# Kernel optimization log

Hardware: AMD Instinct MI355X
Metric: run time of the kernel (lower is better)

## Reference

```python
import jax, jax.numpy as jnp
import numpy as np

B, L, D, N, OUT, NL = 4, 1024, 512, 16, 512, 2  # batch, seq, channels, ssm state, output, layers


def setup_inputs() -> dict:
    key = jax.random.key(0)
    ks = jax.random.split(key, 8)
    sc = D ** -0.5
    return {
        "x": jax.random.normal(ks[0], (B, L, D), jnp.float32),
        # diagonal A: negative real part (real_random=False -> stable negative init)
        "A": -jax.random.uniform(ks[1], (NL, D, N), jnp.float32, 0.1, 1.0),
        "D_skip": jnp.ones((NL, D), jnp.float32),
        "WB": jax.random.normal(ks[2], (NL, D, N), jnp.float32) * sc,
        "bB": jnp.zeros((NL, N), jnp.float32),
        "WC": jax.random.normal(ks[3], (NL, D, N), jnp.float32) * sc,
        "bC": jnp.zeros((NL, N), jnp.float32),
        "Wdt": jax.random.normal(ks[4], (NL, D, D), jnp.float32) * sc,
        "bdt": jnp.full((NL, D), -4.0, jnp.float32),  # softplus(-4) ~ 0.018 -> small dt
        "Wlin": jax.random.normal(ks[5], (NL, D, D), jnp.float32) * sc,
        "blin": jnp.zeros((NL, D), jnp.float32),
        "Wdec": jax.random.normal(ks[6], (D, OUT), jnp.float32) * sc,
        "bdec": jnp.zeros((OUT,), jnp.float32),
    }


def _linear_scan(a, b):
    # first-order linear recurrence h_t = a_t * h_{t-1} + b_t via parallel scan
    def comb(c1, c2):
        a1, b1 = c1
        a2, b2 = c2
        return a1 * a2, a2 * b1 + b2
    return jax.lax.associative_scan(comb, (a, b), axis=1)[1]


def _forward(x, A, D_skip, WB, bB, WC, bC, Wdt, bdt, Wlin, blin, Wdec, bdec):
    y = x
    for i in range(NL):
        # selection mechanism: dt, B, C are input-dependent
        dt = jax.nn.softplus(jnp.einsum('bld,de->ble', y, Wdt[i]) + bdt[i])  # (B,L,D)
        Bm = jnp.einsum('bld,dn->bln', y, WB[i]) + bB[i]                      # (B,L,N)
        Cm = jnp.einsum('bld,dn->bln', y, WC[i]) + bC[i]                      # (B,L,N)
        # ZOH discretization of diagonal SSM
        a = jnp.exp(dt[..., None] * A[i])                                     # (B,L,D,N)
        b = (dt * y)[..., None] * Bm[:, :, None, :]                           # (B,L,D,N)
        h = _linear_scan(a, b)                                                # (B,L,D,N)
        out = jnp.einsum('bldn,bln->bld', h, Cm) + D_skip[i] * y
        y = jnp.maximum(out, 0.0)                                             # ReLU
        y = jnp.einsum('bld,de->ble', y, Wlin[i]) + blin[i]                   # per-layer Linear
    return jnp.einsum('bld,do->blo', y, Wdec) + bdec                          # decoder


def reference(x, A, D_skip, WB, bB, WC, bC, Wdt, bdt, Wlin, blin, Wdec, bdec):
    return _forward(x, A, D_skip, WB, bB, WC, bC, Wdt, bdt, Wlin, blin, Wdec, bdec)
```

## Files before the change

### kernel.cpp

```cpp
#include <hip/hip_runtime.h>

#define BQ 4
#define LQ 1024
#define DQ 512
#define NQ 16
#define MQ (BQ*LQ)
#define CHUNK 16
#define NCH (LQ/CHUNK)
#define KQ 512
#define NFUSE 576

typedef __bf16  bf16x8  __attribute__((ext_vector_type(8)));
typedef float   floatx4 __attribute__((ext_vector_type(4)));

__device__ __forceinline__ float softplus_f(float x) {
    return (x > 20.0f) ? x : log1pf(__expf(x));
}
__device__ __forceinline__ unsigned short f2b(float f) {
    union { float f; unsigned u; } x; x.f = f;
    unsigned r = x.u + 0x7fffu + ((x.u >> 16) & 1u);
    return (unsigned short)(r >> 16);
}
__device__ __forceinline__ float b2f(unsigned short u) {
    union { unsigned u; float f; } x; x.u = (unsigned)u << 16;
    return x.f;
}
__device__ __forceinline__ void load_lds16(const void* g, void* l) {
    __builtin_amdgcn_global_load_lds(
        (const __attribute__((address_space(1))) unsigned int*)g,
        (__attribute__((address_space(3))) unsigned int*)l, 16, 0, 0);
}

__device__ __forceinline__ void stage_tile(
    const unsigned short* g, unsigned short* lds, int wave, int lane)
{
    const int rsub = lane >> 3;
    const int gsrc = (lane & 7) ^ rsub;
    #pragma unroll
    for (int j = 0; j < 2; ++j) {
        int rbase = wave * 16 + j * 8;
        load_lds16(g + (size_t)(rbase + rsub) * KQ + gsrc * 8,
                   lds + (size_t)rbase * 64);
    }
}

__device__ __forceinline__ void gemm_db_core(
    const unsigned short* __restrict__ Abf,
    const unsigned short* __restrict__ Wt,
    int bm, int bn,
    unsigned short (*As)[64*64], unsigned short (*Bs)[64*64],
    floatx4 acc[2][2])
{
    const int lane = threadIdx.x & 63, wave = threadIdx.x >> 6;
    const int mw = (wave & 1) * 32, nw = (wave >> 1) * 32;
    const int r15 = lane & 15, q = lane >> 4;
    const int slot0 = q ^ (r15 & 7);

    #pragma unroll
    for (int i = 0; i < 2; ++i)
        #pragma unroll
        for (int j = 0; j < 2; ++j) acc[i][j] = (floatx4){0.f,0.f,0.f,0.f};

    const unsigned short* ga = Abf + (size_t)bm * KQ;
    const unsigned short* gb = Wt  + (size_t)bn * KQ;
    stage_tile(ga, As[0], wave, lane);
    stage_tile(gb, Bs[0], wave, lane);

    #pragma unroll
    for (int it = 0; it < 8; ++it) {
        __syncthreads();
        if (it < 7) {
            stage_tile(ga + (it + 1) * 64, As[(it + 1) & 1], wave, lane);
            stage_tile(gb + (it + 1) * 64, Bs[(it + 1) & 1], wave, lane);
        }
        const unsigned short* a = As[it & 1];
        const unsigned short* b = Bs[it & 1];
        #pragma unroll
        for (int ks = 0; ks < 2; ++ks) {
            int slot = slot0 ^ (ks * 4);
            bf16x8 af0 = *(const bf16x8*)&a[(mw      + r15) * 64 + slot * 8];
            bf16x8 af1 = *(const bf16x8*)&a[(mw + 16 + r15) * 64 + slot * 8];
            bf16x8 bf0 = *(const bf16x8*)&b[(nw      + r15) * 64 + slot * 8];
            bf16x8 bf1 = *(const bf16x8*)&b[(nw + 16 + r15) * 64 + slot * 8];
            acc[0][0] = __builtin_amdgcn_mfma_f32_16x16x32_bf16(af0, bf0, acc[0][0], 0,0,0);
            acc[1][0] = __builtin_amdgcn_mfma_f32_16x16x32_bf16(af1, bf0, acc[1][0], 0,0,0);
            acc[0][1] = __builtin_amdgcn_mfma_f32_16x16x32_bf16(af0, bf1, acc[0][1], 0,0,0);
            acc[1][1] = __builtin_amdgcn_mfma_f32_16x16x32_bf16(af1, bf1, acc[1][1], 0,0,0);
        }
    }
}

__device__ __forceinline__ void write_fused(
    floatx4 acc[2][2], int bm, int bn_local,
    const float* __restrict__ bias,
    unsigned short* __restrict__ dtb, float* __restrict__ Bm, float* __restrict__ Cm)
{
    const int lane = threadIdx.x & 63, wave = threadIdx.x >> 6;
    const int mw = (wave & 1) * 32, nw = (wave >> 1) * 32;
    const int col0 = lane & 15, rq = lane >> 4;
    #pragma unroll
    for (int nt = 0; nt < 2; ++nt) {
        int nb = bn_local + nw + nt * 16;
        int n  = nb + col0;
        if (nb >= 544) continue;
        float bv = bias[n];
        #pragma unroll
        for (int mt = 0; mt < 2; ++mt)
            #pragma unroll
            for (int r = 0; r < 4; ++r) {
                int m = bm + mw + mt * 16 + rq * 4 + r;
                float v = acc[mt][nt][r] + bv;
                if (nb < 512)      dtb[(size_t)m * DQ + n] = f2b(softplus_f(v));
                else if (nb < 528) Bm[(size_t)m * NQ + (n - 512)] = v;
                else               Cm[(size_t)m * NQ + (n - 528)] = v;
            }
    }
}

__global__ __launch_bounds__(256) void gemm_fused0(
    const unsigned short* __restrict__ Abf,
    const unsigned short* __restrict__ Wt,
    const float* __restrict__ bias,
    unsigned short* __restrict__ dtb, float* __restrict__ Bm, float* __restrict__ Cm)
{
    __shared__ __align__(16) unsigned short As[2][64*64];
    __shared__ __align__(16) unsigned short Bs[2][64*64];
    const int bm = blockIdx.x * 64, bn = blockIdx.y * 64;
    floatx4 acc[2][2];
    gemm_db_core(Abf, Wt, bm, bn, As, Bs, acc);
    write_fused(acc, bm, bn, bias, dtb, Bm, Cm);
}

__global__ __launch_bounds__(256) void gemm_pair(
    const unsigned short* __restrict__ Abf,
    const unsigned short* __restrict__ Wt_lin0,
    const unsigned short* __restrict__ Wcomb1,
    const float* __restrict__ blin0, const float* __restrict__ bcomb1,
    unsigned short* __restrict__ y16b,
    unsigned short* __restrict__ dtb1, float* __restrict__ Bm1, float* __restrict__ Cm1)
{
    __shared__ __align__(16) unsigned short As[2][64*64];
    __shared__ __align__(16) unsigned short Bs[2][64*64];
    const int bm = blockIdx.x * 64;
    const int tile = blockIdx.y;
    floatx4 acc[2][2];
    if (tile < 8) {
        const int bn = tile * 64;
        gemm_db_core(Abf, Wt_lin0, bm, bn, As, Bs, acc);
        const int lane = threadIdx.x & 63, wave = threadIdx.x >> 6;
        const int mw = (wave & 1) * 32, nw = (wave >> 1) * 32;
        const int col0 = lane & 15, rq = lane >> 4;
        #pragma unroll
        for (int nt = 0; nt < 2; ++nt) {
            int n = bn + nw + nt * 16 + col0;
            float bv = blin0[n];
            #pragma unroll
            for (int mt = 0; mt < 2; ++mt)
                #pragma unroll
                for (int r = 0; r < 4; ++r) {
                    int m = bm + mw + mt * 16 + rq * 4 + r;
                    y16b[(size_t)m * DQ + n] = f2b(acc[mt][nt][r] + bv);
                }
        }
    } else {
        const int bn = (tile - 8) * 64;
        gemm_db_core(Abf, Wcomb1, bm, bn, As, Bs, acc);
        write_fused(acc, bm, bn, bcomb1, dtb1, Bm1, Cm1);
    }
}

__global__ __launch_bounds__(256) void gemm_final(
    const unsigned short* __restrict__ Abf,
    const unsigned short* __restrict__ Wt,
    const float* __restrict__ bias,
    float* __restrict__ out)
{
    __shared__ __align__(16) unsigned short As[2][64*64];
    __shared__ __align__(16) unsigned short Bs[2][64*64];
    const int bm = blockIdx.x * 64, bn = blockIdx.y * 64;
    floatx4 acc[2][2];
    gemm_db_core(Abf, Wt, bm, bn, As, Bs, acc);
    const int lane = threadIdx.x & 63, wave = threadIdx.x >> 6;
    const int mw = (wave & 1) * 32, nw = (wave >> 1) * 32;
    const int col0 = lane & 15, rq = lane >> 4;
    #pragma unroll
    for (int nt = 0; nt < 2; ++nt) {
        int n = bn + nw + nt * 16 + col0;
        float bv = bias[n];
        #pragma unroll
        for (int mt = 0; mt < 2; ++mt)
            #pragma unroll
            for (int r = 0; r < 4; ++r) {
                int m = bm + mw + mt * 16 + rq * 4 + r;
                out[(size_t)m * DQ + n] = acc[mt][nt][r] + bv;
            }
    }
}

__global__ __launch_bounds__(256) void prep_all(
    const float* __restrict__ Wdt, const float* __restrict__ Wlin,
    const float* __restrict__ Wdec,
    const float* __restrict__ WB, const float* __restrict__ WC,
    const float* __restrict__ x,
    unsigned short* __restrict__ Wf0, unsigned short* __restrict__ Wf1,
    unsigned short* __restrict__ Wt_lin0, unsigned short* __restrict__ Wdec_t,
    unsigned short* __restrict__ Wlin0_o, unsigned short* __restrict__ Wlin1_o,
    unsigned short* __restrict__ y16)
{
    const int bid = blockIdx.x, tid = threadIdx.x;
    if (bid < 1024) {
        __shared__ float tile[32][33];
        int mat = bid >> 8, t = bid & 255;
        const float* src; unsigned short* dst;
        switch (mat) {
            case 0:  src = Wdt;                  dst = Wf0;     break;
            case 1:  src = Wdt + (size_t)KQ*KQ;  dst = Wf1;     break;
            case 2:  src = Wlin;                 dst = Wt_lin0; break;
            default: src = Wdec;                 dst = Wdec_t;  break;
        }
        int bx = (t & 15) * 32, by = (t >> 4) * 32;
        int tx = tid & 31, ty = tid >> 5;
        #pragma unroll
        for (int i = 0; i < 32; i += 8)
            tile[ty + i][tx] = src[(size_t)(bx + ty + i) * KQ + by + tx];
        __syncthreads();
        #pragma unroll
        for (int i = 0; i < 32; i += 8)
            dst[(size_t)(by + ty + i) * KQ + bx + tx] = f2b(tile[tx][ty + i]);
    } else if (bid < 1536) {
        int q = bid - 1024;
        const float* src = (q < 256) ? Wlin : Wlin + (size_t)KQ*KQ;
        unsigned short* dst = (q < 256) ? Wlin0_o : Wlin1_o;
        size_t i = ((size_t)(q & 255) * 256 + tid) * 4;
        float4 v = *(const float4*)(src + i);
        ushort4 o;
        o.x = f2b(v.x); o.y = f2b(v.y); o.z = f2b(v.z); o.w = f2b(v.w);
        *(ushort4*)(dst + i) = o;
    } else if (bid < 1664) {
        int job = bid - 1536;
        int layer = job >> 6, r = job & 63;
        unsigned short* dst = (layer ? Wf1 : Wf0) + (size_t)(512 + r) * KQ;
        const float* src = nullptr;
        int n = 0;
        if (r < 16)      { src = WB + (size_t)layer * DQ * NQ; n = r; }
        else if (r < 32) { src = WC + (size_t)layer * DQ * NQ; n = r - 16; }
        for (int k = tid; k < KQ; k += 256)
            dst[k] = src ? f2b(src[(size_t)k * NQ + n]) : (unsigned short)0;
    } else {
        size_t i = ((size_t)(bid - 1664) * 256 + tid) * 4;
        float4 v = *(const float4*)(x + i);
        ushort4 o;
        o.x = f2b(v.x); o.y = f2b(v.y); o.z = f2b(v.z); o.w = f2b(v.w);
        *(ushort4*)(y16 + i) = o;
    }
}

__global__ __launch_bounds__(256) void compose(
    const unsigned short* __restrict__ Wf1_t, const unsigned short* __restrict__ Wlin0_o,
    const unsigned short* __restrict__ Wdec_t, const unsigned short* __restrict__ Wlin1_o,
    const float* __restrict__ blin,
    const float* __restrict__ bdt,
    const float* __restrict__ bB, const float* __restrict__ bC,
    const float* __restrict__ bdec,
    unsigned short* __restrict__ Wcomb1, unsigned short* __restrict__ Wdec_comb,
    float* __restrict__ bcomb1, float* __restrict__ bdec_comb)
{
    const int bid = blockIdx.x, tid = threadIdx.x;
    if (bid < 136) {
        __shared__ __align__(16) unsigned short As[2][64*64];
        __shared__ __align__(16) unsigned short Bs[2][64*64];
        const unsigned short *Abf, *Wt; unsigned short* dst;
        int bm, bn;
        if (bid < 72) { Abf = Wf1_t;  Wt = Wlin0_o; dst = Wcomb1;
                        bm = (bid / 8) * 64; bn = (bid % 8) * 64; }
        else          { int q = bid - 72; Abf = Wdec_t; Wt = Wlin1_o; dst = Wdec_comb;
                        bm = (q / 8) * 64; bn = (q % 8) * 64; }
        floatx4 acc[2][2];
        gemm_db_core(Abf, Wt, bm, bn, As, Bs, acc);
        const int lane = tid & 63, wave = tid >> 6;
        const int mw = (wave & 1) * 32, nw = (wave >> 1) * 32;
        const int col0 = lane & 15, rq = lane >> 4;
        #pragma unroll
        for (int nt = 0; nt < 2; ++nt) {
            int n = bn + nw + nt * 16 + col0;
            #pragma unroll
            for (int mt = 0; mt < 2; ++mt)
                #pragma unroll
                for (int r = 0; r < 4; ++r) {
                    int m = bm + mw + mt * 16 + rq * 4 + r;
                    dst[(size_t)m * KQ + n] = f2b(acc[mt][nt][r]);
                }
        }
    } else {
        const int within = tid >> 3, part = tid & 7;
        float acc = 0.f;
        if (bid < 154) {
            int n = (bid - 136) * 32 + within;
            const unsigned short* wrow = Wf1_t + (size_t)n * KQ + part * 64;
            const float* bl = blin;
            #pragma unroll 8
            for (int j = 0; j < 64; ++j)
                acc = fmaf(bl[part * 64 + j], b2f(wrow[j]), acc);
            acc += __shfl_xor(acc, 1);
            acc += __shfl_xor(acc, 2);
            acc += __shfl_xor(acc, 4);
            if (part == 0) {
                float base;
                if (n < 512)      base = bdt[DQ + n];
                else if (n < 528) base = bB[NQ + (n - 512)];
                else if (n < 544) base = bC[NQ + (n - 528)];
                else              base = 0.f;
                bcomb1[n] = acc + base;
            }
        } else {
            int n = (bid - 154) * 32 + within;
            const unsigned short* wrow = Wdec_t + (size_t)n * KQ + part * 64;
            const float* bl = blin + DQ;
            #pragma unroll 8
            for (int j = 0; j < 64; ++j)
                acc = fmaf(bl[part * 64 + j], b2f(wrow[j]), acc);
            acc += __shfl_xor(acc, 1);
            acc += __shfl_xor(acc, 2);
            acc += __shfl_xor(acc, 4);
            if (part == 0) bdec_comb[n] = acc + bdec[n];
        }
    }
}

__global__ __launch_bounds__(256) void build_bias0(
    const float* __restrict__ bdt, const float* __restrict__ bB,
    const float* __restrict__ bC, float* __restrict__ bfused0)
{
    int i = blockIdx.x * 256 + threadIdx.x;
    if (i < 512)      bfused0[i] = bdt[i];
    else if (i < 528) bfused0[i] = bB[i - 512];
    else if (i < 544) bfused0[i] = bC[i - 528];
    else if (i < 576) bfused0[i] = 0.f;
}

__global__ __launch_bounds__(256) void scan_phase1(
    const unsigned short* __restrict__ dt, const unsigned short* __restrict__ y,
    const float* __restrict__ Bm, const float* __restrict__ A,
    float* __restrict__ ap, float* __restrict__ hf)
{
    int idx  = blockIdx.x;
    int dblk = idx & 1;
    int c    = (idx >> 1) & (NCH - 1);
    int b    = idx >> 7;
    int d    = dblk * 256 + threadIdx.x;

    float Ad[NQ];
    const float* Aptr = A + (size_t)d * NQ;
    #pragma unroll
    for (int n = 0; n < NQ; ++n) Ad[n] = Aptr[n];

    float h[NQ], prod[NQ];
    #pragma unroll
    for (int n = 0; n < NQ; ++n) { h[n] = 0.f; prod[n] = 1.f; }

    int t0 = c * CHUNK;
    const unsigned short* dtp = dt + ((size_t)b*LQ + t0) * DQ + d;
    const unsigned short* yp  = y  + ((size_t)b*LQ + t0) * DQ + d;
    const float* bp  = Bm + ((size_t)b*LQ + t0) * NQ;

    #pragma unroll 4
    for (int t = 0; t < CHUNK; ++t) {
        float dtv = b2f(dtp[(size_t)t * DQ]);
        float yv  = b2f(yp[(size_t)t * DQ]);
        float dty = dtv * yv;
        #pragma unroll
        for (int n = 0; n < NQ; ++n) {
            float a = __expf(dtv * Ad[n]);
            prod[n] *= a;
            h[n] = fmaf(a, h[n], dty * bp[t*NQ + n]);
        }
    }
    size_t base = ((size_t)(b*NCH + c) * DQ + d) * NQ;
    #pragma unroll
    for (int n = 0; n < NQ; n += 4) {
        *(float4*)(ap + base + n) = make_float4(prod[n], prod[n+1], prod[n+2], prod[n+3]);
        *(float4*)(hf + base + n) = make_float4(h[n], h[n+1], h[n+2], h[n+3]);
    }
}

__global__ __launch_bounds__(256) void scan_phase2(
    float* ap, const float* __restrict__ hf)
{
    int g = blockIdx.x * 256 + threadIdx.x;
    int n = g & (NQ - 1);
    int d = (g >> 4) & (DQ - 1);
    int b = g >> 13;
    const size_t stride = (size_t)DQ * NQ;
    size_t base = ((size_t)b * NCH * DQ + d) * NQ + n;
    float h = 0.f;
    for (int c0 = 0; c0 < NCH; c0 += 8) {
        float a[8], f[8];
        #pragma unroll
        for (int j = 0; j < 8; ++j) {
            size_t idx = base + (size_t)(c0 + j) * stride;
            a[j] = ap[idx];
            f[j] = hf[idx];
        }
        #pragma unroll
        for (int j = 0; j < 8; ++j) {
            size_t idx = base + (size_t)(c0 + j) * stride;
            ap[idx] = h;
            h = fmaf(a[j], h, f[j]);
        }
    }
}

__global__ __launch_bounds__(256) void scan_phase3(
    const unsigned short* __restrict__ dt, const unsigned short* __restrict__ y,
    const float* __restrict__ Bm, const float* __restrict__ Cm,
    const float* __restrict__ A, const float* __restrict__ Dsk,
    const float* __restrict__ hi, unsigned short* __restrict__ yact)
{
    int idx  = blockIdx.x;
    int dblk = idx & 1;
    int c    = (idx >> 1) & (NCH - 1);
    int b    = idx >> 7;
    int d    = dblk * 256 + threadIdx.x;

    float Ad[NQ];
    const float* Aptr = A + (size_t)d * NQ;
    #pragma unroll
    for (int n = 0; n < NQ; ++n) Ad[n] = Aptr[n];

    float h[NQ];
    size_t base = ((size_t)(b*NCH + c) * DQ + d) * NQ;
    #pragma unroll
    for (int n = 0; n < NQ; n += 4) {
        float4 v = *(const float4*)(hi + base + n);
        h[n] = v.x; h[n+1] = v.y; h[n+2] = v.z; h[n+3] = v.w;
    }
    float dskip = Dsk[d];

    int t0 = c * CHUNK;
    const unsigned short* dtp = dt + ((size_t)b*LQ + t0) * DQ + d;
    const unsigned short* yp  = y  + ((size_t)b*LQ + t0) * DQ + d;
    const float* bp  = Bm + ((size_t)b*LQ + t0) * NQ;
    const float* cp  = Cm + ((size_t)b*LQ + t0) * NQ;
    unsigned short* op = yact + ((size_t)b*LQ + t0) * DQ + d;

    #pragma unroll 4
    for (int t = 0; t < CHUNK; ++t) {
        float dtv = b2f(dtp[(size_t)t * DQ]);
        float yv  = b2f(yp[(size_t)t * DQ]);
        float dty = dtv * yv;
        float acc = 0.f;
        #pragma unroll
        for (int n = 0; n < NQ; ++n) {
            float a = __expf(dtv * Ad[n]);
            h[n] = fmaf(a, h[n], dty * bp[t*NQ + n]);
            acc = fmaf(h[n], cp[t*NQ + n], acc);
        }
        float v = acc + dskip * yv;
        op[(size_t)t * DQ] = f2b(fmaxf(v, 0.f));
    }
}

extern "C" void kernel_launch(void* const* d_in, const int* in_sizes, int n_in,
                              void* d_out, int out_size, void* d_ws, size_t ws_size,
                              hipStream_t stream)
{
    const float* x    = (const float*)d_in[0];
    const float* A    = (const float*)d_in[1];
    const float* Dsk  = (const float*)d_in[2];
    const float* WB   = (const float*)d_in[3];
    const float* bB   = (const float*)d_in[4];
    const float* WC   = (const float*)d_in[5];
    const float* bC   = (const float*)d_in[6];
    const float* Wdt  = (const float*)d_in[7];
    const float* bdt  = (const float*)d_in[8];
    const float* Wlin = (const float*)d_in[9];
    const float* blin = (const float*)d_in[10];
    const float* Wdec = (const float*)d_in[11];
    const float* bdec = (const float*)d_in[12];
    float* out = (float*)d_out;

    char* cur = (char*)d_ws;
    float* Bm0  = (float*)cur;  cur += (size_t)MQ*NQ*4;
    float* Cm0  = (float*)cur;  cur += (size_t)MQ*NQ*4;
    float* Bm1  = (float*)cur;  cur += (size_t)MQ*NQ*4;
    float* Cm1  = (float*)cur;  cur += (size_t)MQ*NQ*4;
    float* ap   = (float*)cur;  cur += (size_t)BQ*NCH*DQ*NQ*4;
    float* hf   = (float*)cur;  cur += (size_t)BQ*NCH*DQ*NQ*4;
    unsigned short* y16    = (unsigned short*)cur; cur += (size_t)MQ*DQ*2;
    unsigned short* y16b   = (unsigned short*)cur; cur += (size_t)MQ*DQ*2;
    unsigned short* dtb0   = (unsigned short*)cur; cur += (size_t)MQ*DQ*2;
    unsigned short* dtb1   = (unsigned short*)cur; cur += (size_t)MQ*DQ*2;
    unsigned short* yact   = (unsigned short*)cur; cur += (size_t)MQ*DQ*2;
    unsigned short* Wf0    = (unsigned short*)cur; cur += (size_t)NFUSE*KQ*2;
    unsigned short* Wf1    = (unsigned short*)cur; cur += (size_t)NFUSE*KQ*2;
    unsigned short* Wt_lin0 = (unsigned short*)cur; cur += (size_t)KQ*KQ*2;
    unsigned short* Wdec_t  = (unsigned short*)cur; cur += (size_t)KQ*KQ*2;
    unsigned short* Wlin0_o = (unsigned short*)cur; cur += (size_t)KQ*KQ*2;
    unsigned short* Wlin1_o = (unsigned short*)cur; cur += (size_t)KQ*KQ*2;
    unsigned short* Wcomb1  = (unsigned short*)cur; cur += (size_t)NFUSE*KQ*2;
    unsigned short* Wdec_comb = (unsigned short*)cur; cur += (size_t)KQ*KQ*2;
    float* bfused0   = (float*)cur;  cur += NFUSE*4;
    float* bcomb1    = (float*)cur;  cur += NFUSE*4;
    float* bdec_comb = (float*)cur;  cur += DQ*4;

    dim3 blk(256);

    prep_all<<<dim3(3712), blk, 0, stream>>>(
        Wdt, Wlin, Wdec, WB, WC, x,
        Wf0, Wf1, Wt_lin0, Wdec_t, Wlin0_o, Wlin1_o, y16);
    build_bias0<<<dim3(3), blk, 0, stream>>>(bdt, bB, bC, bfused0);

    compose<<<dim3(170), blk, 0, stream>>>(
        Wf1, Wlin0_o, Wdec_t, Wlin1_o,
        blin, bdt, bB, bC, bdec,
        Wcomb1, Wdec_comb, bcomb1, bdec_comb);

    gemm_fused0<<<dim3(MQ/64, NFUSE/64), blk, 0, stream>>>(
        y16, Wf0, bfused0, dtb0, Bm0, Cm0);

    scan_phase1<<<dim3(BQ*NCH*2), blk, 0, stream>>>(dtb0, y16, Bm0, A, ap, hf);
    scan_phase2<<<dim3(BQ*DQ*NQ/256), blk, 0, stream>>>(ap, hf);
    scan_phase3<<<dim3(BQ*NCH*2), blk, 0, stream>>>(
        dtb0, y16, Bm0, Cm0, A, Dsk, ap, yact);

    gemm_pair<<<dim3(MQ/64, 17), blk, 0, stream>>>(
        yact, Wt_lin0, Wcomb1, blin, bcomb1, y16b, dtb1, Bm1, Cm1);

    scan_phase1<<<dim3(BQ*NCH*2), blk, 0, stream>>>(
        dtb1, y16b, Bm1, A + (size_t)DQ*NQ, ap, hf);
    scan_phase2<<<dim3(BQ*DQ*NQ/256), blk, 0, stream>>>(ap, hf);
    scan_phase3<<<dim3(BQ*NCH*2), blk, 0, stream>>>(
        dtb1, y16b, Bm1, Cm1, A + (size_t)DQ*NQ, Dsk + DQ, ap, yact);

    gemm_final<<<dim3(MQ/64, DQ/64), blk, 0, stream>>>(
        yact, Wdec_comb, bdec_comb, out);
}
```

Baseline: 201.8 us.

## Stage full-K A tile in LDS and keep B fragments in registers

Replaces the double-buffered 64x64 K-stepping GEMM core with one that loads the whole 64x512 A tile into LDS (64 KB) in a single pass. Each wave loads its B fragments straight from global memory into registers, which removes the per-iteration barriers and the B staging through LDS. It also folds the build_bias0 kernel into the compose kernel to save one launch. In exchange, the larger LDS footprint and the register-held B fragments may reduce occupancy, and there is no overlap between loading and compute.

```diff
diff --git a/kernel.cpp b/kernel.cpp
--- a/kernel.cpp
+++ b/kernel.cpp
@@ -31,62 +31,67 @@
         (__attribute__((address_space(3))) unsigned int*)l, 16, 0, 0);
 }
 
-__device__ __forceinline__ void stage_tile(
-    const unsigned short* g, unsigned short* lds, int wave, int lane)
-{
-    const int rsub = lane >> 3;
-    const int gsrc = (lane & 7) ^ rsub;
-    #pragma unroll
-    for (int j = 0; j < 2; ++j) {
-        int rbase = wave * 16 + j * 8;
-        load_lds16(g + (size_t)(rbase + rsub) * KQ + gsrc * 8,
-                   lds + (size_t)rbase * 64);
-    }
-}
-
-__device__ __forceinline__ void gemm_db_core(
+__device__ __forceinline__ void gemm_ak_core(
     const unsigned short* __restrict__ Abf,
     const unsigned short* __restrict__ Wt,
-    int bm, int bn,
-    unsigned short (*As)[64*64], unsigned short (*Bs)[64*64],
-    floatx4 acc[2][2])
+    int bm, int bn, unsigned short* As, floatx4 acc[2][2])
 {
     const int lane = threadIdx.x & 63, wave = threadIdx.x >> 6;
     const int mw = (wave & 1) * 32, nw = (wave >> 1) * 32;
     const int r15 = lane & 15, q = lane >> 4;
-    const int slot0 = q ^ (r15 & 7);
 
     #pragma unroll
     for (int i = 0; i < 2; ++i)
         #pragma unroll
         for (int j = 0; j < 2; ++j) acc[i][j] = (floatx4){0.f,0.f,0.f,0.f};
 
-    const unsigned short* ga = Abf + (size_t)bm * KQ;
-    const unsigned short* gb = Wt  + (size_t)bn * KQ;
-    stage_tile(ga, As[0], wave, lane);
-    stage_tile(gb, Bs[0], wave, lane);
+    #pragma unroll
+    for (int r = 0; r < 16; ++r) {
+        int row = wave * 16 + r;
+        load_lds16(Abf + (size_t)(bm + row) * KQ + (size_t)((lane ^ (row & 7)) * 8),
+                   As + (size_t)row * KQ);
+    }
+
+    const unsigned short* bp = Wt + (size_t)(bn + nw + r15) * KQ + q * 8;
+    bf16x8 bfr0[8][2], bfr1[8][2];
+    #pragma unroll
+    for (int it = 0; it < 8; ++it)
+        #pragma unroll
+        for (int nt = 0; nt < 2; ++nt)
+            bfr0[it][nt] = *(const bf16x8*)(bp + (size_t)nt * 16 * KQ + it * 32);
+
+    __syncthreads();
+
+    #pragma unroll
+    for (int it = 0; it < 8; ++it)
+        #pragma unroll
+        for (int nt = 0; nt < 2; ++nt)
+            bfr1[it][nt] = *(const bf16x8*)(bp + (size_t)nt * 16 * KQ + 256 + it * 32);
+
+    const int row0 = mw + r15, row1 = mw + 16 + r15;
+    const int sw = r15 & 7;
+    unsigned short* a0 = As + (size_t)row0 * KQ;
+    unsigned short* a1 = As + (size_t)row1 * KQ;
 
     #pragma unroll
     for (int it = 0; it < 8; ++it) {
-        __syncthreads();
-        if (it < 7) {
-            stage_tile(ga + (it + 1) * 64, As[(it + 1) & 1], wave, lane);
-            stage_tile(gb + (it + 1) * 64, Bs[(it + 1) & 1], wave, lane);
-        }
-        const unsigned short* a = As[it & 1];
-        const unsigned short* b = Bs[it & 1];
-        #pragma unroll
-        for (int ks = 0; ks < 2; ++ks) {
-            int slot = slot0 ^ (ks * 4);
-            bf16x8 af0 = *(const bf16x8*)&a[(mw      + r15) * 64 + slot * 8];
-            bf16x8 af1 = *(const bf16x8*)&a[(mw + 16 + r15) * 64 + slot * 8];
-            bf16x8 bf0 = *(const bf16x8*)&b[(nw      + r15) * 64 + slot * 8];
-            bf16x8 bf1 = *(const bf16x8*)&b[(nw + 16 + r15) * 64 + slot * 8];
-            acc[0][0] = __builtin_amdgcn_mfma_f32_16x16x32_bf16(af0, bf0, acc[0][0], 0,0,0);
-            acc[1][0] = __builtin_amdgcn_mfma_f32_16x16x32_bf16(af1, bf0, acc[1][0], 0,0,0);
-            acc[0][1] = __builtin_amdgcn_mfma_f32_16x16x32_bf16(af0, bf1, acc[0][1], 0,0,0);
-            acc[1][1] = __builtin_amdgcn_mfma_f32_16x16x32_bf16(af1, bf1, acc[1][1], 0,0,0);
-        }
+        int g = it * 4 + q;
+        bf16x8 af0 = *(const bf16x8*)(a0 + (g ^ sw) * 8);
+        bf16x8 af1 = *(const bf16x8*)(a1 + (g ^ sw) * 8);
+        acc[0][0] = __builtin_amdgcn_mfma_f32_16x16x32_bf16(af0, bfr0[it][0], acc[0][0], 0,0,0);
+        acc[1][0] = __builtin_amdgcn_mfma_f32_16x16x32_bf16(af1, bfr0[it][0], acc[1][0], 0,0,0);
+        acc[0][1] = __builtin_amdgcn_mfma_f32_16x16x32_bf16(af0, bfr0[it][1], acc[0][1], 0,0,0);
+        acc[1][1] = __builtin_amdgcn_mfma_f32_16x16x32_bf16(af1, bfr0[it][1], acc[1][1], 0,0,0);
+    }
+    #pragma unroll
+    for (int it = 0; it < 8; ++it) {
+        int g = 32 + it * 4 + q;
+        bf16x8 af0 = *(const bf16x8*)(a0 + (g ^ sw) * 8);
+        bf16x8 af1 = *(const bf16x8*)(a1 + (g ^ sw) * 8);
+        acc[0][0] = __builtin_amdgcn_mfma_f32_16x16x32_bf16(af0, bfr1[it][0], acc[0][0], 0,0,0);
+        acc[1][0] = __builtin_amdgcn_mfma_f32_16x16x32_bf16(af1, bfr1[it][0], acc[1][0], 0,0,0);
+        acc[0][1] = __builtin_amdgcn_mfma_f32_16x16x32_bf16(af0, bfr1[it][1], acc[0][1], 0,0,0);
+        acc[1][1] = __builtin_amdgcn_mfma_f32_16x16x32_bf16(af1, bfr1[it][1], acc[1][1], 0,0,0);
     }
 }
 
@@ -123,11 +128,10 @@
     const float* __restrict__ bias,
     unsigned short* __restrict__ dtb, float* __restrict__ Bm, float* __restrict__ Cm)
 {
-    __shared__ __align__(16) unsigned short As[2][64*64];
-    __shared__ __align__(16) unsigned short Bs[2][64*64];
+    __shared__ __align__(16) unsigned short As[64 * KQ];
     const int bm = blockIdx.x * 64, bn = blockIdx.y * 64;
     floatx4 acc[2][2];
-    gemm_db_core(Abf, Wt, bm, bn, As, Bs, acc);
+    gemm_ak_core(Abf, Wt, bm, bn, As, acc);
     write_fused(acc, bm, bn, bias, dtb, Bm, Cm);
 }
 
@@ -139,14 +143,13 @@
     unsigned short* __restrict__ y16b,
     unsigned short* __restrict__ dtb1, float* __restrict__ Bm1, float* __restrict__ Cm1)
 {
-    __shared__ __align__(16) unsigned short As[2][64*64];
-    __shared__ __align__(16) unsigned short Bs[2][64*64];
+    __shared__ __align__(16) unsigned short As[64 * KQ];
     const int bm = blockIdx.x * 64;
     const int tile = blockIdx.y;
     floatx4 acc[2][2];
     if (tile < 8) {
         const int bn = tile * 64;
-        gemm_db_core(Abf, Wt_lin0, bm, bn, As, Bs, acc);
+        gemm_ak_core(Abf, Wt_lin0, bm, bn, As, acc);
         const int lane = threadIdx.x & 63, wave = threadIdx.x >> 6;
         const int mw = (wave & 1) * 32, nw = (wave >> 1) * 32;
         const int col0 = lane & 15, rq = lane >> 4;
@@ -164,7 +167,7 @@
         }
     } else {
         const int bn = (tile - 8) * 64;
-        gemm_db_core(Abf, Wcomb1, bm, bn, As, Bs, acc);
+        gemm_ak_core(Abf, Wcomb1, bm, bn, As, acc);
         write_fused(acc, bm, bn, bcomb1, dtb1, Bm1, Cm1);
     }
 }
@@ -175,11 +178,10 @@
     const float* __restrict__ bias,
     float* __restrict__ out)
 {
-    __shared__ __align__(16) unsigned short As[2][64*64];
-    __shared__ __align__(16) unsigned short Bs[2][64*64];
+    __shared__ __align__(16) unsigned short As[64 * KQ];
     const int bm = blockIdx.x * 64, bn = blockIdx.y * 64;
     floatx4 acc[2][2];
-    gemm_db_core(Abf, Wt, bm, bn, As, Bs, acc);
+    gemm_ak_core(Abf, Wt, bm, bn, As, acc);
     const int lane = threadIdx.x & 63, wave = threadIdx.x >> 6;
     const int mw = (wave & 1) * 32, nw = (wave >> 1) * 32;
     const int col0 = lane & 15, rq = lane >> 4;
@@ -263,12 +265,12 @@
     const float* __restrict__ bB, const float* __restrict__ bC,
     const float* __restrict__ bdec,
     unsigned short* __restrict__ Wcomb1, unsigned short* __restrict__ Wdec_comb,
-    float* __restrict__ bcomb1, float* __restrict__ bdec_comb)
+    float* __restrict__ bcomb1, float* __restrict__ bdec_comb,
+    float* __restrict__ bfused0)
 {
     const int bid = blockIdx.x, tid = threadIdx.x;
     if (bid < 136) {
-        __shared__ __align__(16) unsigned short As[2][64*64];
-        __shared__ __align__(16) unsigned short Bs[2][64*64];
+        __shared__ __align__(16) unsigned short As[64 * KQ];
         const unsigned short *Abf, *Wt; unsigned short* dst;
         int bm, bn;
         if (bid < 72) { Abf = Wf1_t;  Wt = Wlin0_o; dst = Wcomb1;
@@ -276,7 +278,7 @@
         else          { int q = bid - 72; Abf = Wdec_t; Wt = Wlin1_o; dst = Wdec_comb;
                         bm = (q / 8) * 64; bn = (q % 8) * 64; }
         floatx4 acc[2][2];
-        gemm_db_core(Abf, Wt, bm, bn, As, Bs, acc);
+        gemm_ak_core(Abf, Wt, bm, bn, As, acc);
         const int lane = tid & 63, wave = tid >> 6;
         const int mw = (wave & 1) * 32, nw = (wave >> 1) * 32;
         const int col0 = lane & 15, rq = lane >> 4;
@@ -291,7 +293,7 @@
                     dst[(size_t)m * KQ + n] = f2b(acc[mt][nt][r]);
                 }
         }
-    } else {
+    } else if (bid < 170) {
         const int within = tid >> 3, part = tid & 7;
         float acc = 0.f;
         if (bid < 154) {
@@ -324,18 +326,13 @@
             acc += __shfl_xor(acc, 4);
             if (part == 0) bdec_comb[n] = acc + bdec[n];
         }
-    }
-}
-
-__global__ __launch_bounds__(256) void build_bias0(
-    const float* __restrict__ bdt, const float* __restrict__ bB,
-    const float* __restrict__ bC, float* __restrict__ bfused0)
-{
-    int i = blockIdx.x * 256 + threadIdx.x;
-    if (i < 512)      bfused0[i] = bdt[i];
-    else if (i < 528) bfused0[i] = bB[i - 512];
-    else if (i < 544) bfused0[i] = bC[i - 528];
-    else if (i < 576) bfused0[i] = 0.f;
+    } else {
+        int i = (bid - 170) * 256 + tid;
+        if (i < 512)      bfused0[i] = bdt[i];
+        else if (i < 528) bfused0[i] = bB[i - 512];
+        else if (i < 544) bfused0[i] = bC[i - 528];
+        else if (i < 576) bfused0[i] = 0.f;
+    }
 }
 
 __global__ __launch_bounds__(256) void scan_phase1(
@@ -508,12 +505,11 @@
     prep_all<<<dim3(3712), blk, 0, stream>>>(
         Wdt, Wlin, Wdec, WB, WC, x,
         Wf0, Wf1, Wt_lin0, Wdec_t, Wlin0_o, Wlin1_o, y16);
-    build_bias0<<<dim3(3), blk, 0, stream>>>(bdt, bB, bC, bfused0);
-
-    compose<<<dim3(170), blk, 0, stream>>>(
+
+    compose<<<dim3(173), blk, 0, stream>>>(
         Wf1, Wlin0_o, Wdec_t, Wlin1_o,
         blin, bdt, bB, bC, bdec,
-        Wcomb1, Wdec_comb, bcomb1, bdec_comb);
+        Wcomb1, Wdec_comb, bcomb1, bdec_comb, bfused0);
 
     gemm_fused0<<<dim3(MQ/64, NFUSE/64), blk, 0, stream>>>(
         y16, Wf0, bfused0, dtb0, Bm0, Cm0);
```

Result: slower. 221.3 us (+9.7%).

## Merge compose into first GEMM launch, fold bias build, stagger K-tile order

Applied to the files above, without the earlier changes.

Folds the bias-building kernel into prep_all and merges the weight-composition GEMMs and bias reductions into the same launch as the first fused GEMM, cutting two kernel launches and letting the small compose work run alongside the large GEMM. It also adds a per-block stagger of the K-tile traversal order in all GEMMs, so concurrently running blocks read different K slices and contend less on the same memory channels. The staggered order changes the float summation order slightly, and the merged kernel mixes block types with different runtimes.

```diff
diff --git a/kernel.cpp b/kernel.cpp
--- a/kernel.cpp
+++ b/kernel.cpp
@@ -47,7 +47,7 @@
 __device__ __forceinline__ void gemm_db_core(
     const unsigned short* __restrict__ Abf,
     const unsigned short* __restrict__ Wt,
-    int bm, int bn,
+    int bm, int bn, int stag,
     unsigned short (*As)[64*64], unsigned short (*Bs)[64*64],
     floatx4 acc[2][2])
 {
@@ -63,15 +63,19 @@
 
     const unsigned short* ga = Abf + (size_t)bm * KQ;
     const unsigned short* gb = Wt  + (size_t)bn * KQ;
-    stage_tile(ga, As[0], wave, lane);
-    stage_tile(gb, Bs[0], wave, lane);
+    {
+        int kt = (stag & 7) * 64;
+        stage_tile(ga + kt, As[0], wave, lane);
+        stage_tile(gb + kt, Bs[0], wave, lane);
+    }
 
     #pragma unroll
     for (int it = 0; it < 8; ++it) {
         __syncthreads();
         if (it < 7) {
-            stage_tile(ga + (it + 1) * 64, As[(it + 1) & 1], wave, lane);
-            stage_tile(gb + (it + 1) * 64, Bs[(it + 1) & 1], wave, lane);
+            int kt = ((it + 1 + stag) & 7) * 64;
+            stage_tile(ga + kt, As[(it + 1) & 1], wave, lane);
+            stage_tile(gb + kt, Bs[(it + 1) & 1], wave, lane);
         }
         const unsigned short* a = As[it & 1];
         const unsigned short* b = Bs[it & 1];
@@ -117,18 +121,83 @@
     }
 }
 
-__global__ __launch_bounds__(256) void gemm_fused0(
-    const unsigned short* __restrict__ Abf,
-    const unsigned short* __restrict__ Wt,
-    const float* __restrict__ bias,
-    unsigned short* __restrict__ dtb, float* __restrict__ Bm, float* __restrict__ Cm)
+__global__ __launch_bounds__(256) void gemm_f0_compose(
+    const unsigned short* __restrict__ y16,
+    const unsigned short* __restrict__ Wf0, const float* __restrict__ bfused0,
+    unsigned short* __restrict__ dtb0, float* __restrict__ Bm0, float* __restrict__ Cm0,
+    const unsigned short* __restrict__ Wf1_t, const unsigned short* __restrict__ Wlin0_o,
+    const unsigned short* __restrict__ Wdec_t, const unsigned short* __restrict__ Wlin1_o,
+    const float* __restrict__ blin, const float* __restrict__ bdt,
+    const float* __restrict__ bB, const float* __restrict__ bC,
+    const float* __restrict__ bdec,
+    unsigned short* __restrict__ Wcomb1, unsigned short* __restrict__ Wdec_comb,
+    float* __restrict__ bcomb1, float* __restrict__ bdec_comb)
 {
     __shared__ __align__(16) unsigned short As[2][64*64];
     __shared__ __align__(16) unsigned short Bs[2][64*64];
-    const int bm = blockIdx.x * 64, bn = blockIdx.y * 64;
-    floatx4 acc[2][2];
-    gemm_db_core(Abf, Wt, bm, bn, As, Bs, acc);
-    write_fused(acc, bm, bn, bias, dtb, Bm, Cm);
+    const int bid = blockIdx.x, tid = threadIdx.x;
+    if (bid < 576) {
+        const int bm = (bid & 63) * 64, bn = (bid >> 6) * 64;
+        floatx4 acc[2][2];
+        gemm_db_core(y16, Wf0, bm, bn, bid, As, Bs, acc);
+        write_fused(acc, bm, bn, bfused0, dtb0, Bm0, Cm0);
+    } else if (bid < 712) {
+        const unsigned short *Abf, *Wt; unsigned short* dst;
+        int bm, bn;
+        if (bid < 648) { int q = bid - 576; Abf = Wf1_t;  Wt = Wlin0_o; dst = Wcomb1;
+                         bm = (q / 8) * 64; bn = (q % 8) * 64; }
+        else           { int q = bid - 648; Abf = Wdec_t; Wt = Wlin1_o; dst = Wdec_comb;
+                         bm = (q / 8) * 64; bn = (q % 8) * 64; }
+        floatx4 acc[2][2];
+        gemm_db_core(Abf, Wt, bm, bn, bid, As, Bs, acc);
+        const int lane = tid & 63, wave = tid >> 6;
+        const int mw = (wave & 1) * 32, nw = (wave >> 1) * 32;
+        const int col0 = lane & 15, rq = lane >> 4;
+        #pragma unroll
+        for (int nt = 0; nt < 2; ++nt) {
+            int n = bn + nw + nt * 16 + col0;
+            #pragma unroll
+            for (int mt = 0; mt < 2; ++mt)
+                #pragma unroll
+                for (int r = 0; r < 4; ++r) {
+                    int m = bm + mw + mt * 16 + rq * 4 + r;
+                    dst[(size_t)m * KQ + n] = f2b(acc[mt][nt][r]);
+                }
+        }
+    } else {
+        const int within = tid >> 3, part = tid & 7;
+        float acc = 0.f;
+        if (bid < 730) {
+            int n = (bid - 712) * 32 + within;
+            const unsigned short* wrow = Wf1_t + (size_t)n * KQ + part * 64;
+            const float* bl = blin;
+            #pragma unroll 8
+            for (int j = 0; j < 64; ++j)
+                acc = fmaf(bl[part * 64 + j], b2f(wrow[j]), acc);
+            acc += __shfl_xor(acc, 1);
+            acc += __shfl_xor(acc, 2);
+            acc += __shfl_xor(acc, 4);
+            if (part == 0) {
+                float base;
+                if (n < 512)      base = bdt[DQ + n];
+                else if (n < 528) base = bB[NQ + (n - 512)];
+                else if (n < 544) base = bC[NQ + (n - 528)];
+                else              base = 0.f;
+                bcomb1[n] = acc + base;
+            }
+        } else {
+            int n = (bid - 730) * 32 + within;
+            const unsigned short* wrow = Wdec_t + (size_t)n * KQ + part * 64;
+            const float* bl = blin + DQ;
+            #pragma unroll 8
+            for (int j = 0; j < 64; ++j)
+                acc = fmaf(bl[part * 64 + j], b2f(wrow[j]), acc);
+            acc += __shfl_xor(acc, 1);
+            acc += __shfl_xor(acc, 2);
+            acc += __shfl_xor(acc, 4);
+            if (part == 0) bdec_comb[n] = acc + bdec[n];
+        }
+    }
 }
 
 __global__ __launch_bounds__(256) void gemm_pair(
@@ -143,10 +212,11 @@
     __shared__ __align__(16) unsigned short Bs[2][64*64];
     const int bm = blockIdx.x * 64;
     const int tile = blockIdx.y;
+    const int stag = blockIdx.x + blockIdx.y;
     floatx4 acc[2][2];
     if (tile < 8) {
         const int bn = tile * 64;
-        gemm_db_core(Abf, Wt_lin0, bm, bn, As, Bs, acc);
+        gemm_db_core(Abf, Wt_lin0, bm, bn, stag, As, Bs, acc);
         const int lane = threadIdx.x & 63, wave = threadIdx.x >> 6;
         const int mw = (wave & 1) * 32, nw = (wave >> 1) * 32;
         const int col0 = lane & 15, rq = lane >> 4;
@@ -164,7 +234,7 @@
         }
     } else {
         const int bn = (tile - 8) * 64;
-        gemm_db_core(Abf, Wcomb1, bm, bn, As, Bs, acc);
+        gemm_db_core(Abf, Wcomb1, bm, bn, stag, As, Bs, acc);
         write_fused(acc, bm, bn, bcomb1, dtb1, Bm1, Cm1);
     }
 }
@@ -179,7 +249,7 @@
     __shared__ __align__(16) unsigned short Bs[2][64*64];
     const int bm = blockIdx.x * 64, bn = blockIdx.y * 64;
     floatx4 acc[2][2];
-    gemm_db_core(Abf, Wt, bm, bn, As, Bs, acc);
+    gemm_db_core(Abf, Wt, bm, bn, blockIdx.x + blockIdx.y, As, Bs, acc);
     const int lane = threadIdx.x & 63, wave = threadIdx.x >> 6;
     const int mw = (wave & 1) * 32, nw = (wave >> 1) * 32;
     const int col0 = lane & 15, rq = lane >> 4;
@@ -202,10 +272,12 @@
     const float* __restrict__ Wdec,
     const float* __restrict__ WB, const float* __restrict__ WC,
     const float* __restrict__ x,
+    const float* __restrict__ bdt, const float* __restrict__ bB,
+    const float* __restrict__ bC,
     unsigned short* __restrict__ Wf0, unsigned short* __restrict__ Wf1,
     unsigned short* __restrict__ Wt_lin0, unsigned short* __restrict__ Wdec_t,
     unsigned short* __restrict__ Wlin0_o, unsigned short* __restrict__ Wlin1_o,
-    unsigned short* __restrict__ y16)
+    unsigned short* __restrict__ y16, float* __restrict__ bfused0)
 {
     const int bid = blockIdx.x, tid = threadIdx.x;
     if (bid < 1024) {
@@ -246,96 +318,19 @@
         else if (r < 32) { src = WC + (size_t)layer * DQ * NQ; n = r - 16; }
         for (int k = tid; k < KQ; k += 256)
             dst[k] = src ? f2b(src[(size_t)k * NQ + n]) : (unsigned short)0;
-    } else {
+    } else if (bid < 3712) {
         size_t i = ((size_t)(bid - 1664) * 256 + tid) * 4;
         float4 v = *(const float4*)(x + i);
         ushort4 o;
         o.x = f2b(v.x); o.y = f2b(v.y); o.z = f2b(v.z); o.w = f2b(v.w);
         *(ushort4*)(y16 + i) = o;
-    }
-}
-
-__global__ __launch_bounds__(256) void compose(
-    const unsigned short* __restrict__ Wf1_t, const unsigned short* __restrict__ Wlin0_o,
-    const unsigned short* __restrict__ Wdec_t, const unsigned short* __restrict__ Wlin1_o,
-    const float* __restrict__ blin,
-    const float* __restrict__ bdt,
-    const float* __restrict__ bB, const float* __restrict__ bC,
-    const float* __restrict__ bdec,
-    unsigned short* __restrict__ Wcomb1, unsigned short* __restrict__ Wdec_comb,
-    float* __restrict__ bcomb1, float* __restrict__ bdec_comb)
-{
-    const int bid = blockIdx.x, tid = threadIdx.x;
-    if (bid < 136) {
-        __shared__ __align__(16) unsigned short As[2][64*64];
-        __shared__ __align__(16) unsigned short Bs[2][64*64];
-        const unsigned short *Abf, *Wt; unsigned short* dst;
-        int bm, bn;
-        if (bid < 72) { Abf = Wf1_t;  Wt = Wlin0_o; dst = Wcomb1;
-                        bm = (bid / 8) * 64; bn = (bid % 8) * 64; }
-        else          { int q = bid - 72; Abf = Wdec_t; Wt = Wlin1_o; dst = Wdec_comb;
-                        bm = (q / 8) * 64; bn = (q % 8) * 64; }
-        floatx4 acc[2][2];
-        gemm_db_core(Abf, Wt, bm, bn, As, Bs, acc);
-        const int lane = tid & 63, wave = tid >> 6;
-        const int mw = (wave & 1) * 32, nw = (wave >> 1) * 32;
-        const int col0 = lane & 15, rq = lane >> 4;
-        #pragma unroll
-        for (int nt = 0; nt < 2; ++nt) {
-            int n = bn + nw + nt * 16 + col0;
-            #pragma unroll
-            for (int mt = 0; mt < 2; ++mt)
-                #pragma unroll
-                for (int r = 0; r < 4; ++r) {
-                    int m = bm + mw + mt * 16 + rq * 4 + r;
-                    dst[(size_t)m * KQ + n] = f2b(acc[mt][nt][r]);
-                }
-        }
     } else {
-        const int within = tid >> 3, part = tid & 7;
-        float acc = 0.f;
-        if (bid < 154) {
-            int n = (bid - 136) * 32 + within;
-            const unsigned short* wrow = Wf1_t + (size_t)n * KQ + part * 64;
-            const float* bl = blin;
-            #pragma unroll 8
-            for (int j = 0; j < 64; ++j)
-                acc = fmaf(bl[part * 64 + j], b2f(wrow[j]), acc);
-            acc += __shfl_xor(acc, 1);
-            acc += __shfl_xor(acc, 2);
-            acc += __shfl_xor(acc, 4);
-            if (part == 0) {
-                float base;
-                if (n < 512)      base = bdt[DQ + n];
-                else if (n < 528) base = bB[NQ + (n - 512)];
-                else if (n < 544) base = bC[NQ + (n - 528)];
-                else              base = 0.f;
-                bcomb1[n] = acc + base;
-            }
-        } else {
-            int n = (bid - 154) * 32 + within;
-            const unsigned short* wrow = Wdec_t + (size_t)n * KQ + part * 64;
-            const float* bl = blin + DQ;
-            #pragma unroll 8
-            for (int j = 0; j < 64; ++j)
-                acc = fmaf(bl[part * 64 + j], b2f(wrow[j]), acc);
-            acc += __shfl_xor(acc, 1);
-            acc += __shfl_xor(acc, 2);
-            acc += __shfl_xor(acc, 4);
-            if (part == 0) bdec_comb[n] = acc + bdec[n];
-        }
-    }
-}
-
-__global__ __launch_bounds__(256) void build_bias0(
-    const float* __restrict__ bdt, const float* __restrict__ bB,
-    const float* __restrict__ bC, float* __restrict__ bfused0)
-{
-    int i = blockIdx.x * 256 + threadIdx.x;
-    if (i < 512)      bfused0[i] = bdt[i];
-    else if (i < 528) bfused0[i] = bB[i - 512];
-    else if (i < 544) bfused0[i] = bC[i - 528];
-    else if (i < 576) bfused0[i] = 0.f;
+        int i = (bid - 3712) * 256 + tid;
+        if (i < 512)      bfused0[i] = bdt[i];
+        else if (i < 528) bfused0[i] = bB[i - 512];
+        else if (i < 544) bfused0[i] = bC[i - 528];
+        else if (i < 576) bfused0[i] = 0.f;
+    }
 }
 
 __global__ __launch_bounds__(256) void scan_phase1(
@@ -505,18 +500,15 @@
 
     dim3 blk(256);
 
-    prep_all<<<dim3(3712), blk, 0, stream>>>(
-        Wdt, Wlin, Wdec, WB, WC, x,
-        Wf0, Wf1, Wt_lin0, Wdec_t, Wlin0_o, Wlin1_o, y16);
-    build_bias0<<<dim3(3), blk, 0, stream>>>(bdt, bB, bC, bfused0);
-
-    compose<<<dim3(170), blk, 0, stream>>>(
+    prep_all<<<dim3(3715), blk, 0, stream>>>(
+        Wdt, Wlin, Wdec, WB, WC, x, bdt, bB, bC,
+        Wf0, Wf1, Wt_lin0, Wdec_t, Wlin0_o, Wlin1_o, y16, bfused0);
+
+    gemm_f0_compose<<<dim3(746), blk, 0, stream>>>(
+        y16, Wf0, bfused0, dtb0, Bm0, Cm0,
         Wf1, Wlin0_o, Wdec_t, Wlin1_o,
         blin, bdt, bB, bC, bdec,
         Wcomb1, Wdec_comb, bcomb1, bdec_comb);
-
-    gemm_fused0<<<dim3(MQ/64, NFUSE/64), blk, 0, stream>>>(
-        y16, Wf0, bfused0, dtb0, Bm0, Cm0);
 
     scan_phase1<<<dim3(BQ*NCH*2), blk, 0, stream>>>(dtb0, y16, Bm0, A, ap, hf);
     scan_phase2<<<dim3(BQ*DQ*NQ/256), blk, 0, stream>>>(ap, hf);
```

New measurement: 190.9 us. -5.4%, faster.
